# Kernel tuning notes

Hardware: AMD Instinct MI355X
Metric: run time of the kernel (lower is better)

## Reference

```python
import jax, jax.numpy as jnp
import numpy as np
import math

B, L, H, NH = 8, 200, 128, 2
HD = H // NH  # head dim = 64
TIME_VOCAB = 32
LN_EPS = 1e-12


def setup_inputs() -> dict:
    key = jax.random.key(0)
    ks = jax.random.split(key, 16)
    rn = lambda k, shape, s=0.02: (jax.random.normal(k, shape, jnp.float32) * s)
    return {
        "input_tensor": jax.random.normal(ks[0], (B, L, H), jnp.float32),
        "time_seq": jnp.sort(jax.random.randint(ks[1], (B, L), 0, 100000, jnp.int64), axis=-1),
        "attention_mask": jnp.zeros((B, 1, L, L), jnp.float32),
        "Wq": rn(ks[2], (H, H)), "bq": jnp.zeros((H,), jnp.float32),
        "Wk": rn(ks[3], (H, H)), "bk": jnp.zeros((H,), jnp.float32),
        "Wv": rn(ks[4], (H, H)), "bv": jnp.zeros((H,), jnp.float32),
        "Wd": rn(ks[5], (H, H)), "bd": jnp.zeros((H,), jnp.float32),
        "ln_g": jnp.ones((H,), jnp.float32), "ln_b": jnp.zeros((H,), jnp.float32),
        "key_time_table": rn(ks[6], (TIME_VOCAB, H)),
        "value_time_table": rn(ks[7], (TIME_VOCAB, H)),
        "key_pos_table": rn(ks[8], (L, H)),
        "value_pos_table": rn(ks[9], (L, H)),
    }


def _split_heads(x):
    # [B, L, H] -> [B, NH, L, HD]
    b, l, _ = x.shape
    return x.reshape(b, l, NH, HD).transpose(0, 2, 1, 3)


def reference(input_tensor, time_seq, attention_mask,
              Wq, bq, Wk, bk, Wv, bv, Wd, bd, ln_g, ln_b,
              key_time_table, value_time_table, key_pos_table, value_pos_table):
    b, l, h = input_tensor.shape

    # position embeddings (same for all batches)
    kpos = key_pos_table[:l].reshape(l, NH, HD).transpose(1, 0, 2)[None]    # [1,NH,L,HD]
    vpos = value_pos_table[:l].reshape(l, NH, HD).transpose(1, 0, 2)[None]  # [1,NH,L,HD]

    q = _split_heads(input_tensor @ Wq + bq)  # [B,NH,L,HD]
    k = _split_heads(input_tensor @ Wk + bk)
    v = _split_heads(input_tensor @ Wv + bv)

    scores = jnp.einsum('bhqd,bhkd->bhqk', q, k + kpos)

    # time decay: diff[b,i,j] = floor(log(1 + |t_i - t_j|))
    t = time_seq
    diff_idx = jnp.log1p(jnp.abs(t[:, :, None] - t[:, None, :]).astype(jnp.float32)).astype(jnp.int32)  # [B,L,L]

    # [B,L,L,H] -> [B,NH,L,L,HD]
    kt = key_time_table[diff_idx].reshape(b, l, l, NH, HD).transpose(0, 3, 1, 2, 4)
    vt = value_time_table[diff_idx].reshape(b, l, l, NH, HD).transpose(0, 3, 1, 2, 4)

    time_scores = jnp.einsum('bhqd,bhqkd->bhqk', q, kt)

    scores = (scores + time_scores) / math.sqrt(HD)
    scores = scores + attention_mask  # additive mask, broadcast over heads

    probs = jax.nn.softmax(scores, axis=-1)  # attn_dropout is identity in eval

    ctx = jnp.einsum('bhqk,bhkd->bhqd', probs, v + vpos)
    # NOTE: original uses raw (masked, pre-softmax) attention_scores here
    time_ctx = jnp.einsum('bhqk,bhqkd->bhqd', scores, vt)
    ctx = ctx + time_ctx

    ctx = ctx.transpose(0, 2, 1, 3).reshape(b, l, h)  # merge heads
    hidden = ctx @ Wd + bd                            # out_dropout identity in eval

    x = hidden + input_tensor
    mu = x.mean(-1, keepdims=True)
    var = ((x - mu) ** 2).mean(-1, keepdims=True)
    return (x - mu) / jnp.sqrt(var + LN_EPS) * ln_g + ln_b
```

## Files before the change

### kernel.cpp

```cpp
#include <hip/hip_runtime.h>
#include <math.h>

#define B_ 8
#define L_ 200
#define H_ 128
#define NH_ 2
#define HD_ 64
#define LP_ 256
#define TV_ 32
#define RQ_ 8

__global__ __launch_bounds__(128)
void qkv_kernel(const float* __restrict__ X,
                const float* __restrict__ Wq, const float* __restrict__ bq,
                const float* __restrict__ Wk, const float* __restrict__ bk,
                const float* __restrict__ Wv, const float* __restrict__ bv,
                const float* __restrict__ kpt, const float* __restrict__ vpt,
                float* __restrict__ Q, float* __restrict__ Kt, float* __restrict__ Vp){
    const int r0 = blockIdx.x * RQ_;
    const int m  = blockIdx.y;
    const int j  = threadIdx.x;
    __shared__ float xs[RQ_][H_];
    #pragma unroll
    for (int r = 0; r < RQ_; ++r) xs[r][j] = X[(r0 + r) * H_ + j];
    __syncthreads();
    const float* W = (m == 0) ? Wq : ((m == 1) ? Wk : Wv);
    float acc[RQ_];
    #pragma unroll
    for (int r = 0; r < RQ_; ++r) acc[r] = 0.f;
    #pragma unroll 8
    for (int i = 0; i < H_; ++i) {
        const float w = W[i * H_ + j];
        #pragma unroll
        for (int r = 0; r < RQ_; ++r) acc[r] += xs[r][i] * w;
    }
    const int h = j >> 6, d = j & 63;
    if (m == 0) {
        const float bj = bq[j];
        #pragma unroll
        for (int r = 0; r < RQ_; ++r) Q[(r0 + r) * H_ + j] = acc[r] + bj;
    } else if (m == 1) {
        const float bj = bk[j];
        #pragma unroll
        for (int r = 0; r < RQ_; ++r) {
            const int row = r0 + r, b = row / L_, l = row % L_;
            Kt[((b * NH_ + h) * HD_ + d) * LP_ + l] = acc[r] + bj + kpt[l * H_ + j];
        }
    } else {
        const float bj = bv[j];
        #pragma unroll
        for (int r = 0; r < RQ_; ++r) {
            const int row = r0 + r, b = row / L_, l = row % L_;
            Vp[((b * NH_ + h) * L_ + l) * HD_ + d] = acc[r] + bj + vpt[l * H_ + j];
        }
    }
}

__global__ __launch_bounds__(256)
void attn_out_kernel(const float* __restrict__ Q, const float* __restrict__ Kt,
                     const float* __restrict__ Vp, const int* __restrict__ tseq,
                     const float* __restrict__ mask,
                     const float* __restrict__ ktt, const float* __restrict__ vtt,
                     const float* __restrict__ Wd, const float* __restrict__ bd,
                     const float* __restrict__ X, const float* __restrict__ g,
                     const float* __restrict__ bb, float* __restrict__ out){
    const int b  = blockIdx.x / (L_ / 4);
    const int q0 = (blockIdx.x % (L_ / 4)) * 4;
    const int w  = threadIdx.x >> 6, lane = threadIdx.x & 63;
    const int h  = w & 1, qp = w >> 1;
    const int qa = q0 + 2 * qp, qb = qa + 1;
    const int bh = b * NH_ + h;

    __shared__ float ktt_s[TV_][H_ + 1];
    __shared__ float vtt_s[TV_][H_ + 1];
    __shared__ __align__(16) float qs [4][2][HD_];
    __shared__ __align__(16) float qkt[4][2][TV_];
    __shared__ __align__(16) float ss [4][2][TV_];
    __shared__ __align__(16) float ps [4][2][LP_];
    __shared__ __align__(16) float ctx_s[4][H_];
    __shared__ float redA[4], redB[4], red2A[4], red2B[4];

    for (int t = threadIdx.x; t < TV_ * H_; t += 256) {
        ktt_s[t >> 7][t & 127] = ktt[t];
        vtt_s[t >> 7][t & 127] = vtt[t];
    }
    qs[w][0][lane] = Q[(b * L_ + qa) * H_ + h * HD_ + lane];
    qs[w][1][lane] = Q[(b * L_ + qb) * H_ + h * HD_ + lane];
    ss[w][lane >> 5][lane & 31] = 0.f;
    __syncthreads();

    {
        const int i = lane & 31, qsel = lane >> 5;
        float a = 0.f;
        #pragma unroll 8
        for (int d = 0; d < HD_; ++d)
            a += qs[w][qsel][d] * ktt_s[i][h * HD_ + d];
        qkt[w][qsel][i] = a;
    }

    const float4* kt4 = (const float4*)(Kt + (size_t)bh * HD_ * LP_);
    float4 sa = make_float4(0.f, 0.f, 0.f, 0.f);
    float4 sb = make_float4(0.f, 0.f, 0.f, 0.f);
    #pragma unroll 8
    for (int d = 0; d < HD_; ++d) {
        const float4 kv = kt4[d * (LP_ / 4) + lane];
        const float qad = qs[w][0][d], qbd = qs[w][1][d];
        sa.x += qad * kv.x; sa.y += qad * kv.y; sa.z += qad * kv.z; sa.w += qad * kv.w;
        sb.x += qbd * kv.x; sb.y += qbd * kv.y; sb.z += qbd * kv.z; sb.w += qbd * kv.w;
    }
    float sva[4] = {sa.x, sa.y, sa.z, sa.w};
    float svb[4] = {sb.x, sb.y, sb.z, sb.w};
    const int k0i = lane * 4;
    float mxa = -INFINITY, mxb = -INFINITY;
    if (k0i < L_) {
        const float4 m4a = ((const float4*)(mask + ((size_t)(b * L_ + qa)) * L_))[lane];
        const float4 m4b = ((const float4*)(mask + ((size_t)(b * L_ + qb)) * L_))[lane];
        const int4   t4  = ((const int4*)(tseq + b * L_))[lane];
        const int    tqa = tseq[b * L_ + qa], tqb = tseq[b * L_ + qb];
        const float mva[4] = {m4a.x, m4a.y, m4a.z, m4a.w};
        const float mvb[4] = {m4b.x, m4b.y, m4b.z, m4b.w};
        const int   tk[4]  = {t4.x, t4.y, t4.z, t4.w};
        #pragma unroll
        for (int jj = 0; jj < 4; ++jj) {
            int dta = tqa - tk[jj]; if (dta < 0) dta = -dta;
            int dtb = tqb - tk[jj]; if (dtb < 0) dtb = -dtb;
            int ia = (int)log1pf((float)dta); if (ia > TV_ - 1) ia = TV_ - 1;
            int ib = (int)log1pf((float)dtb); if (ib > TV_ - 1) ib = TV_ - 1;
            float s_a = (sva[jj] + qkt[w][0][ia]) * 0.125f + mva[jj];
            float s_b = (svb[jj] + qkt[w][1][ib]) * 0.125f + mvb[jj];
            sva[jj] = s_a; svb[jj] = s_b;
            atomicAdd(&ss[w][0][ia], s_a);
            atomicAdd(&ss[w][1][ib], s_b);
            if (s_a > mxa) mxa = s_a;
            if (s_b > mxb) mxb = s_b;
        }
    } else {
        sva[0] = sva[1] = sva[2] = sva[3] = -INFINITY;
        svb[0] = svb[1] = svb[2] = svb[3] = -INFINITY;
    }
    for (int off = 32; off; off >>= 1) {
        float oa = __shfl_xor(mxa, off); if (oa > mxa) mxa = oa;
        float ob = __shfl_xor(mxb, off); if (ob > mxb) mxb = ob;
    }
    float suma = 0.f, sumb = 0.f, eva[4], evb[4];
    #pragma unroll
    for (int jj = 0; jj < 4; ++jj) {
        float ea = (k0i + jj < L_) ? __expf(sva[jj] - mxa) : 0.f;
        float eb = (k0i + jj < L_) ? __expf(svb[jj] - mxb) : 0.f;
        eva[jj] = ea; suma += ea;
        evb[jj] = eb; sumb += eb;
    }
    for (int off = 32; off; off >>= 1) { suma += __shfl_xor(suma, off); sumb += __shfl_xor(sumb, off); }
    ((float4*)ps[w][0])[lane] = make_float4(eva[0], eva[1], eva[2], eva[3]);
    ((float4*)ps[w][1])[lane] = make_float4(evb[0], evb[1], evb[2], evb[3]);

    const float inva = 1.f / suma, invb = 1.f / sumb;
    const float* vp = Vp + (size_t)bh * L_ * HD_;
    const float4* psa4 = (const float4*)ps[w][0];
    const float4* psb4 = (const float4*)ps[w][1];
    float ca = 0.f, cb = 0.f;
    #pragma unroll 5
    for (int k4 = 0; k4 < L_ / 4; ++k4) {
        const float4 pa = psa4[k4], pb = psb4[k4];
        const int kb = k4 * 4;
        const float v0 = vp[(kb + 0) * HD_ + lane];
        const float v1 = vp[(kb + 1) * HD_ + lane];
        const float v2 = vp[(kb + 2) * HD_ + lane];
        const float v3 = vp[(kb + 3) * HD_ + lane];
        ca += pa.x * v0; ca += pa.y * v1; ca += pa.z * v2; ca += pa.w * v3;
        cb += pb.x * v0; cb += pb.y * v1; cb += pb.z * v2; cb += pb.w * v3;
    }
    ca *= inva; cb *= invb;
    float tca = 0.f, tcb = 0.f;
    const float4* ssa4 = (const float4*)ss[w][0];
    const float4* ssb4 = (const float4*)ss[w][1];
    #pragma unroll
    for (int i4 = 0; i4 < TV_ / 4; ++i4) {
        const float4 za = ssa4[i4], zb = ssb4[i4];
        const int i = i4 * 4;
        const float w0 = vtt_s[i + 0][h * HD_ + lane];
        const float w1 = vtt_s[i + 1][h * HD_ + lane];
        const float w2 = vtt_s[i + 2][h * HD_ + lane];
        const float w3 = vtt_s[i + 3][h * HD_ + lane];
        tca += za.x * w0; tca += za.y * w1; tca += za.z * w2; tca += za.w * w3;
        tcb += zb.x * w0; tcb += zb.y * w1; tcb += zb.z * w2; tcb += zb.w * w3;
    }
    ctx_s[2 * qp + 0][h * HD_ + lane] = ca + tca;
    ctx_s[2 * qp + 1][h * HD_ + lane] = cb + tcb;
    __syncthreads();

    const int r = threadIdx.x >> 7, j = threadIdx.x & 127;
    const float4* ca4 = (const float4*)ctx_s[r];
    const float4* cb4 = (const float4*)ctx_s[r + 2];
    float acc_a = 0.f, acc_b = 0.f;
    #pragma unroll 8
    for (int i4 = 0; i4 < H_ / 4; ++i4) {
        const float4 xa = ca4[i4], xb = cb4[i4];
        const int i = i4 * 4;
        const float w0 = Wd[(i + 0) * H_ + j];
        const float w1 = Wd[(i + 1) * H_ + j];
        const float w2 = Wd[(i + 2) * H_ + j];
        const float w3 = Wd[(i + 3) * H_ + j];
        acc_a += xa.x * w0; acc_a += xa.y * w1; acc_a += xa.z * w2; acc_a += xa.w * w3;
        acc_b += xb.x * w0; acc_b += xb.y * w1; acc_b += xb.z * w2; acc_b += xb.w * w3;
    }
    const int rowa = b * L_ + q0 + r, rowb = rowa + 2;
    const float bdj = bd[j];
    const float x_a = acc_a + bdj + X[rowa * H_ + j];
    const float x_b = acc_b + bdj + X[rowb * H_ + j];

    float s1a = x_a, s1b = x_b;
    for (int off = 32; off; off >>= 1) { s1a += __shfl_xor(s1a, off); s1b += __shfl_xor(s1b, off); }
    if (lane == 0) { redA[w] = s1a; redB[w] = s1b; }
    __syncthreads();
    const float meanA = (redA[2 * r] + redA[2 * r + 1]) * (1.f / H_);
    const float meanB = (redB[2 * r] + redB[2 * r + 1]) * (1.f / H_);
    const float dxa = x_a - meanA, dxb = x_b - meanB;
    float s2a = dxa * dxa, s2b = dxb * dxb;
    for (int off = 32; off; off >>= 1) { s2a += __shfl_xor(s2a, off); s2b += __shfl_xor(s2b, off); }
    if (lane == 0) { red2A[w] = s2a; red2B[w] = s2b; }
    __syncthreads();
    const float varA = (red2A[2 * r] + red2A[2 * r + 1]) * (1.f / H_);
    const float varB = (red2B[2 * r] + red2B[2 * r + 1]) * (1.f / H_);
    const float gj = g[j], bbj = bb[j];
    out[rowa * H_ + j] = dxa * rsqrtf(varA + 1e-12f) * gj + bbj;
    out[rowb * H_ + j] = dxb * rsqrtf(varB + 1e-12f) * gj + bbj;
}

extern "C" void kernel_launch(void* const* d_in, const int* in_sizes, int n_in,
                              void* d_out, int out_size, void* d_ws, size_t ws_size,
                              hipStream_t stream) {
    const float* X    = (const float*)d_in[0];
    const int*   tseq = (const int*)  d_in[1];
    const float* mask = (const float*)d_in[2];
    const float* Wq = (const float*)d_in[3],  *bq = (const float*)d_in[4];
    const float* Wk = (const float*)d_in[5],  *bk = (const float*)d_in[6];
    const float* Wv = (const float*)d_in[7],  *bv = (const float*)d_in[8];
    const float* Wd = (const float*)d_in[9],  *bd = (const float*)d_in[10];
    const float* g  = (const float*)d_in[11], *bb = (const float*)d_in[12];
    const float* ktt = (const float*)d_in[13], *vtt = (const float*)d_in[14];
    const float* kpt = (const float*)d_in[15], *vpt = (const float*)d_in[16];

    float* ws  = (float*)d_ws;
    float* Q   = ws;
    float* Kt  = Q   + B_ * L_ * H_;
    float* Vp  = Kt  + B_ * NH_ * HD_ * LP_;

    dim3 g1(B_ * L_ / RQ_, 3);
    qkv_kernel<<<g1, 128, 0, stream>>>(X, Wq, bq, Wk, bk, Wv, bv, kpt, vpt, Q, Kt, Vp);
    attn_out_kernel<<<B_ * (L_ / 4), 256, 0, stream>>>(Q, Kt, Vp, tseq, mask, ktt, vtt,
                                                       Wd, bd, X, g, bb, (float*)d_out);
}
```

Baseline: 118.8 us.

## Use one wave per query-head in attention kernel and vectorize QKV inner loop

The attention/output kernel grows from 256 to 512 threads per block, so each wavefront handles one query-head pair instead of two. The ctx reduction is redone with float4 V loads split across lane groups and combined by shuffles. LayerNorm now takes E[x^2]-mean^2 in a single reduction pass, removing one barrier. The QKV kernel reads x from shared memory as float4 with four weights per step. The aim is more parallelism and fewer serial steps per wave, at the cost of larger blocks, reading K/V tiles twice as often per query pair, and slightly less stable variance arithmetic.

```diff
diff --git a/kernel.cpp b/kernel.cpp
--- a/kernel.cpp
+++ b/kernel.cpp
@@ -20,7 +20,7 @@
     const int r0 = blockIdx.x * RQ_;
     const int m  = blockIdx.y;
     const int j  = threadIdx.x;
-    __shared__ float xs[RQ_][H_];
+    __shared__ __align__(16) float xs[RQ_][H_];
     #pragma unroll
     for (int r = 0; r < RQ_; ++r) xs[r][j] = X[(r0 + r) * H_ + j];
     __syncthreads();
@@ -28,11 +28,18 @@
     float acc[RQ_];
     #pragma unroll
     for (int r = 0; r < RQ_; ++r) acc[r] = 0.f;
-    #pragma unroll 8
-    for (int i = 0; i < H_; ++i) {
-        const float w = W[i * H_ + j];
-        #pragma unroll
-        for (int r = 0; r < RQ_; ++r) acc[r] += xs[r][i] * w;
+    #pragma unroll 2
+    for (int i4 = 0; i4 < H_ / 4; ++i4) {
+        const int i = i4 * 4;
+        const float w0 = W[(i + 0) * H_ + j];
+        const float w1 = W[(i + 1) * H_ + j];
+        const float w2 = W[(i + 2) * H_ + j];
+        const float w3 = W[(i + 3) * H_ + j];
+        #pragma unroll
+        for (int r = 0; r < RQ_; ++r) {
+            const float4 xv = ((const float4*)xs[r])[i4];
+            acc[r] += xv.x * w0 + xv.y * w1 + xv.z * w2 + xv.w * w3;
+        }
     }
     const int h = j >> 6, d = j & 63;
     if (m == 0) {
@@ -56,7 +63,7 @@
     }
 }
 
-__global__ __launch_bounds__(256)
+__global__ __launch_bounds__(512)
 void attn_out_kernel(const float* __restrict__ Q, const float* __restrict__ Kt,
                      const float* __restrict__ Vp, const int* __restrict__ tseq,
                      const float* __restrict__ mask,
@@ -67,164 +74,140 @@
     const int b  = blockIdx.x / (L_ / 4);
     const int q0 = (blockIdx.x % (L_ / 4)) * 4;
     const int w  = threadIdx.x >> 6, lane = threadIdx.x & 63;
-    const int h  = w & 1, qp = w >> 1;
-    const int qa = q0 + 2 * qp, qb = qa + 1;
+    const int h  = w & 1, qr = w >> 1;
+    const int q  = q0 + qr;
     const int bh = b * NH_ + h;
 
     __shared__ float ktt_s[TV_][H_ + 1];
     __shared__ float vtt_s[TV_][H_ + 1];
-    __shared__ __align__(16) float qs [4][2][HD_];
-    __shared__ __align__(16) float qkt[4][2][TV_];
-    __shared__ __align__(16) float ss [4][2][TV_];
-    __shared__ __align__(16) float ps [4][2][LP_];
+    __shared__ __align__(16) float qs   [4][2][HD_];
+    __shared__ float qkt_s[8][TV_];
+    __shared__ float ss_s [8][TV_];
+    __shared__ __align__(16) float ps_s [8][LP_];
     __shared__ __align__(16) float ctx_s[4][H_];
-    __shared__ float redA[4], redB[4], red2A[4], red2B[4];
-
-    for (int t = threadIdx.x; t < TV_ * H_; t += 256) {
+    __shared__ float redA[8], redB[8];
+
+    for (int t = threadIdx.x; t < TV_ * H_; t += 512) {
         ktt_s[t >> 7][t & 127] = ktt[t];
         vtt_s[t >> 7][t & 127] = vtt[t];
     }
-    qs[w][0][lane] = Q[(b * L_ + qa) * H_ + h * HD_ + lane];
-    qs[w][1][lane] = Q[(b * L_ + qb) * H_ + h * HD_ + lane];
-    ss[w][lane >> 5][lane & 31] = 0.f;
+    qs[qr][h][lane] = Q[(b * L_ + q) * H_ + h * HD_ + lane];
+    if (lane < TV_) ss_s[w][lane] = 0.f;
     __syncthreads();
 
     {
-        const int i = lane & 31, qsel = lane >> 5;
+        const int bkt = lane >> 1, half = lane & 1;
+        const float* kr = &ktt_s[bkt][h * HD_ + half * 32];
+        const float* qv = &qs[qr][h][half * 32];
         float a = 0.f;
-        #pragma unroll 8
-        for (int d = 0; d < HD_; ++d)
-            a += qs[w][qsel][d] * ktt_s[i][h * HD_ + d];
-        qkt[w][qsel][i] = a;
+        #pragma unroll
+        for (int d2 = 0; d2 < 32; ++d2) a += qv[d2] * kr[d2];
+        a += __shfl_xor(a, 1);
+        if (half == 0) qkt_s[w][bkt] = a;
     }
 
     const float4* kt4 = (const float4*)(Kt + (size_t)bh * HD_ * LP_);
-    float4 sa = make_float4(0.f, 0.f, 0.f, 0.f);
-    float4 sb = make_float4(0.f, 0.f, 0.f, 0.f);
-    #pragma unroll 8
-    for (int d = 0; d < HD_; ++d) {
-        const float4 kv = kt4[d * (LP_ / 4) + lane];
-        const float qad = qs[w][0][d], qbd = qs[w][1][d];
-        sa.x += qad * kv.x; sa.y += qad * kv.y; sa.z += qad * kv.z; sa.w += qad * kv.w;
-        sb.x += qbd * kv.x; sb.y += qbd * kv.y; sb.z += qbd * kv.z; sb.w += qbd * kv.w;
-    }
-    float sva[4] = {sa.x, sa.y, sa.z, sa.w};
-    float svb[4] = {sb.x, sb.y, sb.z, sb.w};
+    const float4* qv4 = (const float4*)qs[qr][h];
+    float4 s4 = make_float4(0.f, 0.f, 0.f, 0.f);
+    #pragma unroll 4
+    for (int d4 = 0; d4 < HD_ / 4; ++d4) {
+        const float4 qq = qv4[d4];
+        const float4 k0 = kt4[(d4 * 4 + 0) * (LP_ / 4) + lane];
+        const float4 k1 = kt4[(d4 * 4 + 1) * (LP_ / 4) + lane];
+        const float4 k2 = kt4[(d4 * 4 + 2) * (LP_ / 4) + lane];
+        const float4 k3 = kt4[(d4 * 4 + 3) * (LP_ / 4) + lane];
+        s4.x += qq.x * k0.x + qq.y * k1.x + qq.z * k2.x + qq.w * k3.x;
+        s4.y += qq.x * k0.y + qq.y * k1.y + qq.z * k2.y + qq.w * k3.y;
+        s4.z += qq.x * k0.z + qq.y * k1.z + qq.z * k2.z + qq.w * k3.z;
+        s4.w += qq.x * k0.w + qq.y * k1.w + qq.z * k2.w + qq.w * k3.w;
+    }
+    float sv[4] = {s4.x, s4.y, s4.z, s4.w};
     const int k0i = lane * 4;
-    float mxa = -INFINITY, mxb = -INFINITY;
+    float mx = -INFINITY;
     if (k0i < L_) {
-        const float4 m4a = ((const float4*)(mask + ((size_t)(b * L_ + qa)) * L_))[lane];
-        const float4 m4b = ((const float4*)(mask + ((size_t)(b * L_ + qb)) * L_))[lane];
-        const int4   t4  = ((const int4*)(tseq + b * L_))[lane];
-        const int    tqa = tseq[b * L_ + qa], tqb = tseq[b * L_ + qb];
-        const float mva[4] = {m4a.x, m4a.y, m4a.z, m4a.w};
-        const float mvb[4] = {m4b.x, m4b.y, m4b.z, m4b.w};
-        const int   tk[4]  = {t4.x, t4.y, t4.z, t4.w};
+        const float4 m4 = ((const float4*)(mask + ((size_t)(b * L_ + q)) * L_))[lane];
+        const int4   t4 = ((const int4*)(tseq + b * L_))[lane];
+        const int    tq = tseq[b * L_ + q];
+        const float mv[4] = {m4.x, m4.y, m4.z, m4.w};
+        const int   tk[4] = {t4.x, t4.y, t4.z, t4.w};
         #pragma unroll
         for (int jj = 0; jj < 4; ++jj) {
-            int dta = tqa - tk[jj]; if (dta < 0) dta = -dta;
-            int dtb = tqb - tk[jj]; if (dtb < 0) dtb = -dtb;
-            int ia = (int)log1pf((float)dta); if (ia > TV_ - 1) ia = TV_ - 1;
-            int ib = (int)log1pf((float)dtb); if (ib > TV_ - 1) ib = TV_ - 1;
-            float s_a = (sva[jj] + qkt[w][0][ia]) * 0.125f + mva[jj];
-            float s_b = (svb[jj] + qkt[w][1][ib]) * 0.125f + mvb[jj];
-            sva[jj] = s_a; svb[jj] = s_b;
-            atomicAdd(&ss[w][0][ia], s_a);
-            atomicAdd(&ss[w][1][ib], s_b);
-            if (s_a > mxa) mxa = s_a;
-            if (s_b > mxb) mxb = s_b;
+            int dt = tq - tk[jj]; if (dt < 0) dt = -dt;
+            int ib = (int)log1pf((float)dt); if (ib > TV_ - 1) ib = TV_ - 1;
+            const float s = (sv[jj] + qkt_s[w][ib]) * 0.125f + mv[jj];
+            sv[jj] = s;
+            atomicAdd(&ss_s[w][ib], s);
+            if (s > mx) mx = s;
         }
     } else {
-        sva[0] = sva[1] = sva[2] = sva[3] = -INFINITY;
-        svb[0] = svb[1] = svb[2] = svb[3] = -INFINITY;
-    }
-    for (int off = 32; off; off >>= 1) {
-        float oa = __shfl_xor(mxa, off); if (oa > mxa) mxa = oa;
-        float ob = __shfl_xor(mxb, off); if (ob > mxb) mxb = ob;
-    }
-    float suma = 0.f, sumb = 0.f, eva[4], evb[4];
+        sv[0] = sv[1] = sv[2] = sv[3] = -INFINITY;
+    }
+    #pragma unroll
+    for (int off = 32; off; off >>= 1) { const float o = __shfl_xor(mx, off); if (o > mx) mx = o; }
+    float sum = 0.f, ev[4];
     #pragma unroll
     for (int jj = 0; jj < 4; ++jj) {
-        float ea = (k0i + jj < L_) ? __expf(sva[jj] - mxa) : 0.f;
-        float eb = (k0i + jj < L_) ? __expf(svb[jj] - mxb) : 0.f;
-        eva[jj] = ea; suma += ea;
-        evb[jj] = eb; sumb += eb;
-    }
-    for (int off = 32; off; off >>= 1) { suma += __shfl_xor(suma, off); sumb += __shfl_xor(sumb, off); }
-    ((float4*)ps[w][0])[lane] = make_float4(eva[0], eva[1], eva[2], eva[3]);
-    ((float4*)ps[w][1])[lane] = make_float4(evb[0], evb[1], evb[2], evb[3]);
-
-    const float inva = 1.f / suma, invb = 1.f / sumb;
-    const float* vp = Vp + (size_t)bh * L_ * HD_;
-    const float4* psa4 = (const float4*)ps[w][0];
-    const float4* psb4 = (const float4*)ps[w][1];
-    float ca = 0.f, cb = 0.f;
-    #pragma unroll 5
-    for (int k4 = 0; k4 < L_ / 4; ++k4) {
-        const float4 pa = psa4[k4], pb = psb4[k4];
-        const int kb = k4 * 4;
-        const float v0 = vp[(kb + 0) * HD_ + lane];
-        const float v1 = vp[(kb + 1) * HD_ + lane];
-        const float v2 = vp[(kb + 2) * HD_ + lane];
-        const float v3 = vp[(kb + 3) * HD_ + lane];
-        ca += pa.x * v0; ca += pa.y * v1; ca += pa.z * v2; ca += pa.w * v3;
-        cb += pb.x * v0; cb += pb.y * v1; cb += pb.z * v2; cb += pb.w * v3;
-    }
-    ca *= inva; cb *= invb;
-    float tca = 0.f, tcb = 0.f;
-    const float4* ssa4 = (const float4*)ss[w][0];
-    const float4* ssb4 = (const float4*)ss[w][1];
-    #pragma unroll
-    for (int i4 = 0; i4 < TV_ / 4; ++i4) {
-        const float4 za = ssa4[i4], zb = ssb4[i4];
-        const int i = i4 * 4;
-        const float w0 = vtt_s[i + 0][h * HD_ + lane];
-        const float w1 = vtt_s[i + 1][h * HD_ + lane];
-        const float w2 = vtt_s[i + 2][h * HD_ + lane];
-        const float w3 = vtt_s[i + 3][h * HD_ + lane];
-        tca += za.x * w0; tca += za.y * w1; tca += za.z * w2; tca += za.w * w3;
-        tcb += zb.x * w0; tcb += zb.y * w1; tcb += zb.z * w2; tcb += zb.w * w3;
-    }
-    ctx_s[2 * qp + 0][h * HD_ + lane] = ca + tca;
-    ctx_s[2 * qp + 1][h * HD_ + lane] = cb + tcb;
-    __syncthreads();
-
-    const int r = threadIdx.x >> 7, j = threadIdx.x & 127;
-    const float4* ca4 = (const float4*)ctx_s[r];
-    const float4* cb4 = (const float4*)ctx_s[r + 2];
-    float acc_a = 0.f, acc_b = 0.f;
+        const float e = (k0i + jj < L_) ? __expf(sv[jj] - mx) : 0.f;
+        ev[jj] = e; sum += e;
+    }
+    #pragma unroll
+    for (int off = 32; off; off >>= 1) sum += __shfl_xor(sum, off);
+    ((float4*)ps_s[w])[lane] = make_float4(ev[0], ev[1], ev[2], ev[3]);
+    const float inv = 1.f / sum;
+
+    {
+        const int kk = lane >> 4, d4 = lane & 15;
+        const float4* vp4 = (const float4*)(Vp + (size_t)bh * L_ * HD_);
+        float4 c4 = make_float4(0.f, 0.f, 0.f, 0.f);
+        #pragma unroll 5
+        for (int kb = 0; kb < L_; kb += 4) {
+            const float  p  = ps_s[w][kb + kk];
+            const float4 vv = vp4[(kb + kk) * (HD_ / 4) + d4];
+            c4.x += p * vv.x; c4.y += p * vv.y; c4.z += p * vv.z; c4.w += p * vv.w;
+        }
+        #pragma unroll
+        for (int off = 16; off <= 32; off <<= 1) {
+            c4.x += __shfl_xor(c4.x, off);
+            c4.y += __shfl_xor(c4.y, off);
+            c4.z += __shfl_xor(c4.z, off);
+            c4.w += __shfl_xor(c4.w, off);
+        }
+        if (kk == 0) {
+            c4.x *= inv; c4.y *= inv; c4.z *= inv; c4.w *= inv;
+            *(float4*)&ctx_s[qr][h * HD_ + d4 * 4] = c4;
+        }
+    }
+    {
+        float tc = 0.f;
+        #pragma unroll
+        for (int i = 0; i < TV_; ++i) tc += ss_s[w][i] * vtt_s[i][h * HD_ + lane];
+        ctx_s[qr][h * HD_ + lane] += tc;
+    }
+    __syncthreads();
+
+    const int rr = threadIdx.x >> 7, j = threadIdx.x & 127;
+    const float4* cr = (const float4*)ctx_s[rr];
+    float acc = 0.f;
     #pragma unroll 8
     for (int i4 = 0; i4 < H_ / 4; ++i4) {
-        const float4 xa = ca4[i4], xb = cb4[i4];
+        const float4 xa = cr[i4];
         const int i = i4 * 4;
-        const float w0 = Wd[(i + 0) * H_ + j];
-        const float w1 = Wd[(i + 1) * H_ + j];
-        const float w2 = Wd[(i + 2) * H_ + j];
-        const float w3 = Wd[(i + 3) * H_ + j];
-        acc_a += xa.x * w0; acc_a += xa.y * w1; acc_a += xa.z * w2; acc_a += xa.w * w3;
-        acc_b += xb.x * w0; acc_b += xb.y * w1; acc_b += xb.z * w2; acc_b += xb.w * w3;
-    }
-    const int rowa = b * L_ + q0 + r, rowb = rowa + 2;
-    const float bdj = bd[j];
-    const float x_a = acc_a + bdj + X[rowa * H_ + j];
-    const float x_b = acc_b + bdj + X[rowb * H_ + j];
-
-    float s1a = x_a, s1b = x_b;
-    for (int off = 32; off; off >>= 1) { s1a += __shfl_xor(s1a, off); s1b += __shfl_xor(s1b, off); }
-    if (lane == 0) { redA[w] = s1a; redB[w] = s1b; }
-    __syncthreads();
-    const float meanA = (redA[2 * r] + redA[2 * r + 1]) * (1.f / H_);
-    const float meanB = (redB[2 * r] + redB[2 * r + 1]) * (1.f / H_);
-    const float dxa = x_a - meanA, dxb = x_b - meanB;
-    float s2a = dxa * dxa, s2b = dxb * dxb;
-    for (int off = 32; off; off >>= 1) { s2a += __shfl_xor(s2a, off); s2b += __shfl_xor(s2b, off); }
-    if (lane == 0) { red2A[w] = s2a; red2B[w] = s2b; }
-    __syncthreads();
-    const float varA = (red2A[2 * r] + red2A[2 * r + 1]) * (1.f / H_);
-    const float varB = (red2B[2 * r] + red2B[2 * r + 1]) * (1.f / H_);
-    const float gj = g[j], bbj = bb[j];
-    out[rowa * H_ + j] = dxa * rsqrtf(varA + 1e-12f) * gj + bbj;
-    out[rowb * H_ + j] = dxb * rsqrtf(varB + 1e-12f) * gj + bbj;
+        acc += xa.x * Wd[(i + 0) * H_ + j];
+        acc += xa.y * Wd[(i + 1) * H_ + j];
+        acc += xa.z * Wd[(i + 2) * H_ + j];
+        acc += xa.w * Wd[(i + 3) * H_ + j];
+    }
+    const int row = b * L_ + q0 + rr;
+    const float x = acc + bd[j] + X[row * H_ + j];
+    float s1 = x, s2 = x * x;
+    #pragma unroll
+    for (int off = 32; off; off >>= 1) { s1 += __shfl_xor(s1, off); s2 += __shfl_xor(s2, off); }
+    if (lane == 0) { redA[w] = s1; redB[w] = s2; }
+    __syncthreads();
+    const float mean = (redA[2 * rr] + redA[2 * rr + 1]) * (1.f / H_);
+    const float ex2  = (redB[2 * rr] + redB[2 * rr + 1]) * (1.f / H_);
+    const float var  = ex2 - mean * mean;
+    out[row * H_ + j] = (x - mean) * rsqrtf(var + 1e-12f) * g[j] + bb[j];
 }
 
 extern "C" void kernel_launch(void* const* d_in, const int* in_sizes, int n_in,
@@ -248,6 +231,6 @@
 
     dim3 g1(B_ * L_ / RQ_, 3);
     qkv_kernel<<<g1, 128, 0, stream>>>(X, Wq, bq, Wk, bk, Wv, bv, kpt, vpt, Q, Kt, Vp);
-    attn_out_kernel<<<B_ * (L_ / 4), 256, 0, stream>>>(Q, Kt, Vp, tseq, mask, ktt, vtt,
+    attn_out_kernel<<<B_ * (L_ / 4), 512, 0, stream>>>(Q, Kt, Vp, tseq, mask, ktt, vtt,
                                                        Wd, bd, X, g, bb, (float*)d_out);
 }
```

Measured after the change: 122.6 us. 1.03x slower.
